# Optimization experiments

Hardware: AMD Instinct MI355X
Metric: run time of the kernel (lower is better)

The kernel has to match this reference:

```python
import jax, jax.numpy as jnp
import numpy as np

H = 16          # num_heads
WIN = 256       # window_size

def setup_inputs() -> dict:
    key = jax.random.key(0)
    k1, k2, k3, k4 = jax.random.split(key, 4)
    B, N, C = 2, 4096, 1024
    x = jax.random.normal(k1, (B, N, C), dtype=jnp.float32)
    w_qkv = jax.random.normal(k2, (C, 3 * C), dtype=jnp.float32) * 0.02
    w_proj = jax.random.normal(k3, (C, C), dtype=jnp.float32) * 0.02
    b_proj = jax.random.normal(k4, (C,), dtype=jnp.float32) * 0.02
    return {"x": x, "w_qkv": w_qkv, "w_proj": w_proj, "b_proj": b_proj}

def reference(x, w_qkv, w_proj, b_proj):
    B, N, C = x.shape
    D = C // H
    scale = D ** -0.5
    b = WIN // 2            # block size = half window radius; window = [i-b, i+b]
    nb = N // b             # number of query blocks (N divisible by b here)

    qkv = (x @ w_qkv).reshape(B, N, 3, H, D).transpose(2, 0, 3, 1, 4)  # [3,B,H,N,D]
    q, k, v = qkv[0], qkv[1], qkv[2]                                   # [B,H,N,D]

    qb = q.reshape(B, H, nb, b, D)                                     # [B,H,nb,b,D]
    # pad keys/values by one block on each side, gather 3-block windows
    kp = jnp.pad(k, ((0, 0), (0, 0), (b, b), (0, 0)))                  # [B,H,N+2b,D]
    vp = jnp.pad(v, ((0, 0), (0, 0), (b, b), (0, 0)))
    win_idx = jnp.arange(nb)[:, None] * b + jnp.arange(3 * b)[None, :]  # [nb,3b]
    kw = kp[:, :, win_idx]                                             # [B,H,nb,3b,D]
    vw = vp[:, :, win_idx]

    scores = jnp.einsum('bhnqd,bhnkd->bhnqk', qb, kw) * scale          # [B,H,nb,b,3b]

    # mask: key global pos = j*b + ki - b ; query global pos = j*b + qi
    qi = jnp.arange(b)[:, None]           # [b,1]
    ki = jnp.arange(3 * b)[None, :]       # [1,3b]
    rel_ok = jnp.abs(ki - b - qi) <= b    # [b,3b]  |key - query| <= W/2
    key_pos = (jnp.arange(nb)[:, None] * b + jnp.arange(3 * b)[None, :]) - b  # [nb,3b]
    in_range = (key_pos >= 0) & (key_pos < N)                          # [nb,3b]
    valid = rel_ok[None, :, :] & in_range[:, None, :]                  # [nb,b,3b]

    scores = jnp.where(valid[None, None], scores, -jnp.inf)
    attn = jax.nn.softmax(scores, axis=-1)
    out = jnp.einsum('bhnqk,bhnkd->bhnqd', attn, vw)                   # [B,H,nb,b,D]
    out = out.reshape(B, H, N, D).transpose(0, 2, 1, 3).reshape(B, N, C)
    return out @ w_proj + b_proj
```

## Files before the change

### kernel.cpp

```cpp
#include <hip/hip_runtime.h>

typedef unsigned short ushort_t;
typedef __attribute__((ext_vector_type(8))) short short8;
typedef __attribute__((ext_vector_type(8))) unsigned short ushort8;
typedef __attribute__((ext_vector_type(4))) float f32x4;

__device__ __forceinline__ ushort_t f2bf(float f) {
  union { float f; unsigned int u; } x; x.f = f;
  unsigned int r = x.u + 0x7fffu + ((x.u >> 16) & 1u);
  return (ushort_t)(r >> 16);
}

__device__ __forceinline__ void async16(const void* g, void* lds_uniform) {
  __builtin_amdgcn_global_load_lds(
      (const __attribute__((address_space(1))) void*)g,
      (__attribute__((address_space(3))) void*)lds_uniform, 16, 0, 0);
}

__global__ void conv_x(const float* __restrict__ in, ushort_t* __restrict__ o, int n4) {
  int i = blockIdx.x * blockDim.x + threadIdx.x;
  if (i < n4) {
    float4 f = ((const float4*)in)[i];
    typedef __attribute__((ext_vector_type(4))) unsigned short us4;
    us4 u;
    u[0] = f2bf(f.x); u[1] = f2bf(f.y); u[2] = f2bf(f.z); u[3] = f2bf(f.w);
    ((us4*)o)[i] = u;
  }
}

__global__ void transpose_conv(const float* __restrict__ in, ushort_t* __restrict__ out,
                               int R, int Cc) {
  __shared__ float tile[32][33];
  const int bx = blockIdx.x * 32;
  const int by = blockIdx.y * 32;
  const int tx = threadIdx.x, ty = threadIdx.y;
  #pragma unroll
  for (int i = ty; i < 32; i += 8)
    tile[i][tx] = in[(size_t)(by + i) * Cc + bx + tx];
  __syncthreads();
  #pragma unroll
  for (int i = ty; i < 32; i += 8)
    out[(size_t)(bx + i) * R + by + tx] = f2bf(tile[tx][i]);
}

template<int MODE>
__global__ __launch_bounds__(256) void gemm128(
    const ushort_t* __restrict__ A, const ushort_t* __restrict__ Bt,
    ushort_t* __restrict__ o0, ushort_t* __restrict__ o1, ushort_t* __restrict__ o2,
    const float* __restrict__ bias, float* __restrict__ fout)
{
  constexpr int K = 1024;
  __shared__ __align__(16) ushort_t As[128 * 64];
  __shared__ __align__(16) ushort_t Bs[128 * 64];
  const int tm = blockIdx.y * 128;
  const int tn = blockIdx.x * 128;
  const int tid = threadIdx.x;
  const int w = tid >> 6, lane = tid & 63;
  const int wr = (w >> 1) * 64, wc = (w & 1) * 64;
  const int l15 = lane & 15, lq = lane >> 4;

  const int srow = lane >> 3;
  const int scol = ((lane & 7) ^ srow) << 3;

  const int offk0 = (lq ^ (l15 & 7)) << 4;
  const int offk1 = ((4 + lq) ^ (l15 & 7)) << 4;
  const char* aRd = (const char*)As + (size_t)(wr + l15) * 128;
  const char* bRd = (const char*)Bs + (size_t)(wc + l15) * 128;

  f32x4 acc[4][4] = {};

  for (int k0 = 0; k0 < K; k0 += 64) {
    #pragma unroll
    for (int j = 0; j < 4; ++j) {
      const int c = w * 4 + j;
      const int row = c * 8 + srow;
      async16(A  + (size_t)(tm + row) * K + k0 + scol, (char*)As + c * 1024);
      async16(Bt + (size_t)(tn + row) * K + k0 + scol, (char*)Bs + c * 1024);
    }
    __syncthreads();
    #pragma unroll
    for (int kk = 0; kk < 2; ++kk) {
      const int offk = kk ? offk1 : offk0;
      short8 af[4], bfr[4];
      #pragma unroll
      for (int i = 0; i < 4; ++i) {
        af[i]  = *(const short8*)(aRd + i * 2048 + offk);
        bfr[i] = *(const short8*)(bRd + i * 2048 + offk);
      }
      #pragma unroll
      for (int i = 0; i < 4; ++i)
        #pragma unroll
        for (int j = 0; j < 4; ++j)
          acc[i][j] = __builtin_amdgcn_mfma_f32_16x16x32_bf16(af[i], bfr[j], acc[i][j], 0, 0, 0);
    }
    __syncthreads();
  }

  if (MODE == 0) {
    #pragma unroll
    for (int j = 0; j < 4; ++j) {
      const int col = tn + wc + j * 16 + l15;
      const int which = col >> 10;
      const int h = (col >> 6) & 15, d = col & 63;
      ushort_t* dst = (which == 0) ? o0 : ((which == 1) ? o1 : o2);
      #pragma unroll
      for (int i = 0; i < 4; ++i)
        #pragma unroll
        for (int r = 0; r < 4; ++r) {
          const int m = tm + wr + i * 16 + lq * 4 + r;
          const int b = m >> 12, n = m & 4095;
          dst[(size_t)((b * 16 + h) * 4096 + n) * 64 + d] = f2bf(acc[i][j][r]);
        }
    }
  } else {
    #pragma unroll
    for (int j = 0; j < 4; ++j) {
      const int col = tn + wc + j * 16 + l15;
      const float bv = bias[col];
      #pragma unroll
      for (int i = 0; i < 4; ++i)
        #pragma unroll
        for (int r = 0; r < 4; ++r) {
          const int m = tm + wr + i * 16 + lq * 4 + r;
          fout[(size_t)m * 1024 + col] = acc[i][j][r] + bv;
        }
    }
  }
}

__global__ __launch_bounds__(256) void swin_attn(
    const ushort_t* __restrict__ qb, const ushort_t* __restrict__ kb,
    const ushort_t* __restrict__ vb, ushort_t* __restrict__ attn_out)
{
  constexpr int N = 4096;
  __shared__ __align__(16) ushort_t Ks[64 * 64];
  __shared__ __align__(16) ushort_t VT[64 * 72];
  __shared__ __align__(16) ushort_t Pw[4][32 * 72];
  const int qblk = blockIdx.x;
  const int bh = blockIdx.y;
  const int tid = threadIdx.x;
  const int w = tid >> 6, lane = tid & 63;
  const int l15 = lane & 15, lq = lane >> 4;
  const size_t base = (size_t)bh * N * 64;
  const int q0 = qblk * 128 + w * 32;

  const int offk0 = (lq ^ (l15 & 7)) << 4;
  const int offk1 = ((4 + lq) ^ (l15 & 7)) << 4;
  const int srow = lane >> 3;
  const int scol = ((lane & 7) ^ srow) << 3;

  short8 qf[2][2];
  #pragma unroll
  for (int fm = 0; fm < 2; ++fm)
    #pragma unroll
    for (int kk = 0; kk < 2; ++kk)
      qf[fm][kk] = *(const short8*)&qb[base + (size_t)(q0 + fm * 16 + l15) * 64 + kk * 32 + lq * 8];

  const short ones_bf = (short)0x3F80;
  const short8 ones8 = short8{ones_bf, ones_bf, ones_bf, ones_bf,
                              ones_bf, ones_bf, ones_bf, ones_bf};

  f32x4 oacc[2][5] = {};

  for (int t = 0; t < 6; ++t) {
    const int kpos0 = qblk * 128 - 128 + t * 64;
    if (kpos0 + 63 < 0 || kpos0 >= N) continue;
    const bool active = (kpos0 <= q0 + 31 + 128) && (kpos0 + 63 >= q0 - 128);
    __syncthreads();
    #pragma unroll
    for (int j = 0; j < 2; ++j) {
      const int c = w * 2 + j;
      const int row = c * 8 + srow;
      int kp = kpos0 + row; kp = kp < 0 ? 0 : (kp > N - 1 ? N - 1 : kp);
      async16(kb + base + (size_t)kp * 64 + scol, (char*)Ks + c * 1024);
    }
    {
      const int key = tid >> 2;
      const int dbase = (tid & 3) * 16;
      int kp = kpos0 + key; kp = kp < 0 ? 0 : (kp > N - 1 ? N - 1 : kp);
      const ushort_t* src = vb + base + (size_t)kp * 64 + dbase;
      ushort8 v0 = *(const ushort8*)src;
      ushort8 v1 = *(const ushort8*)(src + 8);
      #pragma unroll
      for (int i = 0; i < 8; ++i) VT[(dbase + i) * 72 + key] = v0[i];
      #pragma unroll
      for (int i = 0; i < 8; ++i) VT[(dbase + 8 + i) * 72 + key] = v1[i];
    }
    __syncthreads();
    if (!active) continue;

    f32x4 sacc[2][4] = {};
    #pragma unroll
    for (int kk = 0; kk < 2; ++kk) {
      const int offk = kk ? offk1 : offk0;
      short8 kf[4];
      #pragma unroll
      for (int fn = 0; fn < 4; ++fn)
        kf[fn] = *(const short8*)((const char*)Ks + (fn * 16 + l15) * 128 + offk);
      #pragma unroll
      for (int fm = 0; fm < 2; ++fm)
        #pragma unroll
        for (int fn = 0; fn < 4; ++fn)
          sacc[fm][fn] = __builtin_amdgcn_mfma_f32_16x16x32_bf16(qf[fm][kk], kf[fn], sacc[fm][fn], 0, 0, 0);
    }

    int kposl[4]; bool inr[4];
    #pragma unroll
    for (int fn = 0; fn < 4; ++fn) {
      kposl[fn] = kpos0 + fn * 16 + l15;
      inr[fn] = (kposl[fn] >= 0) && (kposl[fn] < N);
    }
    #pragma unroll
    for (int fm = 0; fm < 2; ++fm) {
      #pragma unroll
      for (int r = 0; r < 4; ++r) {
        const int qpos = q0 + fm * 16 + lq * 4 + r;
        #pragma unroll
        for (int fn = 0; fn < 4; ++fn) {
          const int dd = kposl[fn] - qpos;
          const bool valid = inr[fn] && (dd <= 128) && (dd >= -128);
          const float p = valid ? __expf(sacc[fm][fn][r] * 0.125f) : 0.f;
          Pw[w][(fm * 16 + lq * 4 + r) * 72 + fn * 16 + l15] = f2bf(p);
        }
      }
    }

    #pragma unroll
    for (int kk = 0; kk < 2; ++kk) {
      short8 pf[2], vf[4];
      #pragma unroll
      for (int fm = 0; fm < 2; ++fm)
        pf[fm] = *(const short8*)&Pw[w][(fm * 16 + l15) * 72 + kk * 32 + lq * 8];
      #pragma unroll
      for (int fn = 0; fn < 4; ++fn)
        vf[fn] = *(const short8*)&VT[(fn * 16 + l15) * 72 + kk * 32 + lq * 8];
      #pragma unroll
      for (int fm = 0; fm < 2; ++fm) {
        #pragma unroll
        for (int fn = 0; fn < 4; ++fn)
          oacc[fm][fn] = __builtin_amdgcn_mfma_f32_16x16x32_bf16(pf[fm], vf[fn], oacc[fm][fn], 0, 0, 0);
        oacc[fm][4] = __builtin_amdgcn_mfma_f32_16x16x32_bf16(pf[fm], ones8, oacc[fm][4], 0, 0, 0);
      }
    }
  }

  const int b = bh >> 4, h = bh & 15;
  #pragma unroll
  for (int fm = 0; fm < 2; ++fm)
    #pragma unroll
    for (int r = 0; r < 4; ++r) {
      const float inv = 1.0f / oacc[fm][4][r];
      const int qpos = q0 + fm * 16 + lq * 4 + r;
      #pragma unroll
      for (int fn = 0; fn < 4; ++fn) {
        const int d = fn * 16 + l15;
        attn_out[(size_t)(b * 4096 + qpos) * 1024 + h * 64 + d] = f2bf(oacc[fm][fn][r] * inv);
      }
    }
}

extern "C" void kernel_launch(void* const* d_in, const int* in_sizes, int n_in,
                              void* d_out, int out_size, void* d_ws, size_t ws_size,
                              hipStream_t stream) {
  const float* x      = (const float*)d_in[0];
  const float* w_qkv  = (const float*)d_in[1];
  const float* w_proj = (const float*)d_in[2];
  const float* b_proj = (const float*)d_in[3];
  float* out = (float*)d_out;
  char* ws = (char*)d_ws;

  ushort_t* x16    = (ushort_t*)(ws);
  ushort_t* wqkvT  = (ushort_t*)(ws + 16777216);
  ushort_t* wprojT = (ushort_t*)(ws + 23068672);
  ushort_t* qbuf   = (ushort_t*)(ws + 25165824);
  ushort_t* kbuf   = (ushort_t*)(ws + 41943040);
  ushort_t* vbuf   = (ushort_t*)(ws + 58720256);
  ushort_t* attn16 = x16;

  conv_x<<<dim3(8192), dim3(256), 0, stream>>>(x, x16, 2097152);
  transpose_conv<<<dim3(96, 32), dim3(32, 8), 0, stream>>>(w_qkv, wqkvT, 1024, 3072);
  transpose_conv<<<dim3(32, 32), dim3(32, 8), 0, stream>>>(w_proj, wprojT, 1024, 1024);
  gemm128<0><<<dim3(24, 64), dim3(256), 0, stream>>>(x16, wqkvT, qbuf, kbuf, vbuf, nullptr, nullptr);
  swin_attn<<<dim3(32, 32), dim3(256), 0, stream>>>(qbuf, kbuf, vbuf, attn16);
  gemm128<1><<<dim3(8, 64), dim3(256), 0, stream>>>(attn16, wprojT, nullptr, nullptr, nullptr, b_proj, out);
}
```

Measured before the change: 142.3 us.

## Store V transposed from QKV GEMM and async-load it directly into LDS

The QKV GEMM epilogue now writes V in a [b,h,d,n] layout instead of [b,h,n,d]. The attention kernel can then stream V^T tiles into LDS with swizzled global_load_lds, matching the K path, instead of doing register loads plus scalar transposed LDS stores. The now-unneeded key clamping and in-range mask checks are dropped, since only fully in-range tiles are processed. The cost is a less coalesced, strided scatter in the GEMM epilogue for the V third of the output.

```diff
diff --git a/kernel.cpp b/kernel.cpp
--- a/kernel.cpp
+++ b/kernel.cpp
@@ -102,14 +102,19 @@
       const int col = tn + wc + j * 16 + l15;
       const int which = col >> 10;
       const int h = (col >> 6) & 15, d = col & 63;
-      ushort_t* dst = (which == 0) ? o0 : ((which == 1) ? o1 : o2);
       #pragma unroll
       for (int i = 0; i < 4; ++i)
         #pragma unroll
         for (int r = 0; r < 4; ++r) {
           const int m = tm + wr + i * 16 + lq * 4 + r;
           const int b = m >> 12, n = m & 4095;
-          dst[(size_t)((b * 16 + h) * 4096 + n) * 64 + d] = f2bf(acc[i][j][r]);
+          const ushort_t val = f2bf(acc[i][j][r]);
+          if (which == 2) {
+            o2[(size_t)((b * 16 + h) * 64 + d) * 4096 + n] = val;
+          } else {
+            ushort_t* dst = (which == 0) ? o0 : o1;
+            dst[(size_t)((b * 16 + h) * 4096 + n) * 64 + d] = val;
+          }
         }
     }
   } else {
@@ -130,11 +135,11 @@
 
 __global__ __launch_bounds__(256) void swin_attn(
     const ushort_t* __restrict__ qb, const ushort_t* __restrict__ kb,
-    const ushort_t* __restrict__ vb, ushort_t* __restrict__ attn_out)
+    const ushort_t* __restrict__ vt, ushort_t* __restrict__ attn_out)
 {
   constexpr int N = 4096;
   __shared__ __align__(16) ushort_t Ks[64 * 64];
-  __shared__ __align__(16) ushort_t VT[64 * 72];
+  __shared__ __align__(16) ushort_t VT[64 * 64];
   __shared__ __align__(16) ushort_t Pw[4][32 * 72];
   const int qblk = blockIdx.x;
   const int bh = blockIdx.y;
@@ -142,6 +147,7 @@
   const int w = tid >> 6, lane = tid & 63;
   const int l15 = lane & 15, lq = lane >> 4;
   const size_t base = (size_t)bh * N * 64;
+  const size_t vtbase = (size_t)bh * 64 * N;
   const int q0 = qblk * 128 + w * 32;
 
   const int offk0 = (lq ^ (l15 & 7)) << 4;
@@ -171,20 +177,8 @@
     for (int j = 0; j < 2; ++j) {
       const int c = w * 2 + j;
       const int row = c * 8 + srow;
-      int kp = kpos0 + row; kp = kp < 0 ? 0 : (kp > N - 1 ? N - 1 : kp);
-      async16(kb + base + (size_t)kp * 64 + scol, (char*)Ks + c * 1024);
-    }
-    {
-      const int key = tid >> 2;
-      const int dbase = (tid & 3) * 16;
-      int kp = kpos0 + key; kp = kp < 0 ? 0 : (kp > N - 1 ? N - 1 : kp);
-      const ushort_t* src = vb + base + (size_t)kp * 64 + dbase;
-      ushort8 v0 = *(const ushort8*)src;
-      ushort8 v1 = *(const ushort8*)(src + 8);
-      #pragma unroll
-      for (int i = 0; i < 8; ++i) VT[(dbase + i) * 72 + key] = v0[i];
-      #pragma unroll
-      for (int i = 0; i < 8; ++i) VT[(dbase + 8 + i) * 72 + key] = v1[i];
+      async16(kb + base + (size_t)(kpos0 + row) * 64 + scol, (char*)Ks + c * 1024);
+      async16(vt + vtbase + (size_t)row * N + kpos0 + scol, (char*)VT + c * 1024);
     }
     __syncthreads();
     if (!active) continue;
@@ -204,12 +198,6 @@
           sacc[fm][fn] = __builtin_amdgcn_mfma_f32_16x16x32_bf16(qf[fm][kk], kf[fn], sacc[fm][fn], 0, 0, 0);
     }
 
-    int kposl[4]; bool inr[4];
-    #pragma unroll
-    for (int fn = 0; fn < 4; ++fn) {
-      kposl[fn] = kpos0 + fn * 16 + l15;
-      inr[fn] = (kposl[fn] >= 0) && (kposl[fn] < N);
-    }
     #pragma unroll
     for (int fm = 0; fm < 2; ++fm) {
       #pragma unroll
@@ -217,8 +205,8 @@
         const int qpos = q0 + fm * 16 + lq * 4 + r;
         #pragma unroll
         for (int fn = 0; fn < 4; ++fn) {
-          const int dd = kposl[fn] - qpos;
-          const bool valid = inr[fn] && (dd <= 128) && (dd >= -128);
+          const int dd = kpos0 + fn * 16 + l15 - qpos;
+          const bool valid = (dd <= 128) && (dd >= -128);
           const float p = valid ? __expf(sacc[fm][fn][r] * 0.125f) : 0.f;
           Pw[w][(fm * 16 + lq * 4 + r) * 72 + fn * 16 + l15] = f2bf(p);
         }
@@ -227,13 +215,14 @@
 
     #pragma unroll
     for (int kk = 0; kk < 2; ++kk) {
+      const int offk = kk ? offk1 : offk0;
       short8 pf[2], vf[4];
       #pragma unroll
       for (int fm = 0; fm < 2; ++fm)
         pf[fm] = *(const short8*)&Pw[w][(fm * 16 + l15) * 72 + kk * 32 + lq * 8];
       #pragma unroll
       for (int fn = 0; fn < 4; ++fn)
-        vf[fn] = *(const short8*)&VT[(fn * 16 + l15) * 72 + kk * 32 + lq * 8];
+        vf[fn] = *(const short8*)((const char*)VT + (fn * 16 + l15) * 128 + offk);
       #pragma unroll
       for (int fm = 0; fm < 2; ++fm) {
         #pragma unroll
@@ -274,13 +263,13 @@
   ushort_t* wprojT = (ushort_t*)(ws + 23068672);
   ushort_t* qbuf   = (ushort_t*)(ws + 25165824);
   ushort_t* kbuf   = (ushort_t*)(ws + 41943040);
-  ushort_t* vbuf   = (ushort_t*)(ws + 58720256);
+  ushort_t* vbufT  = (ushort_t*)(ws + 58720256);
   ushort_t* attn16 = x16;
 
   conv_x<<<dim3(8192), dim3(256), 0, stream>>>(x, x16, 2097152);
   transpose_conv<<<dim3(96, 32), dim3(32, 8), 0, stream>>>(w_qkv, wqkvT, 1024, 3072);
   transpose_conv<<<dim3(32, 32), dim3(32, 8), 0, stream>>>(w_proj, wprojT, 1024, 1024);
-  gemm128<0><<<dim3(24, 64), dim3(256), 0, stream>>>(x16, wqkvT, qbuf, kbuf, vbuf, nullptr, nullptr);
-  swin_attn<<<dim3(32, 32), dim3(256), 0, stream>>>(qbuf, kbuf, vbuf, attn16);
+  gemm128<0><<<dim3(24, 64), dim3(256), 0, stream>>>(x16, wqkvT, qbuf, kbuf, vbufT, nullptr, nullptr);
+  swin_attn<<<dim3(32, 32), dim3(256), 0, stream>>>(qbuf, kbuf, vbufT, attn16);
   gemm128<1><<<dim3(8, 64), dim3(256), 0, stream>>>(attn16, wprojT, nullptr, nullptr, nullptr, b_proj, out);
 }
```

Result: slower. 169.4 us (+19.1%).
